# Kernel optimization log

Hardware: AMD Instinct MI355X
Metric: run time of the kernel (lower is better)

The kernel has to match this reference:

```python
import jax, jax.numpy as jnp
import numpy as np
import math

B, S, DIM = 2, 2048, 4096
N_HEADS, N_KV = 32, 8
HD = DIM // N_HEADS           # 128
N_REP = N_HEADS // N_KV       # 4
MAX_SEQ = 2048


def _rope_freqs(seq_len, head_dim):
    inv = 1.0 / (10000.0 ** (np.arange(0, head_dim, 2, dtype=np.float32) / head_dim))
    ang = np.outer(np.arange(seq_len, dtype=np.float32), inv)  # [S, HD/2]
    return jnp.asarray(np.cos(ang)), jnp.asarray(np.sin(ang))


def setup_inputs() -> dict:
    key = jax.random.key(0)
    ks = jax.random.split(key, 5)
    x = jax.random.normal(ks[0], (B, S, DIM), dtype=jnp.float32)
    wq = jax.random.normal(ks[1], (DIM, N_HEADS * HD), dtype=jnp.float32) * 0.02
    wk = jax.random.normal(ks[2], (DIM, N_KV * HD), dtype=jnp.float32) * 0.02
    wv = jax.random.normal(ks[3], (DIM, N_KV * HD), dtype=jnp.float32) * 0.02
    wo = jax.random.normal(ks[4], (N_HEADS * HD, DIM), dtype=jnp.float32) * 0.02
    freqs_cos, freqs_sin = _rope_freqs(S, HD)
    return {"x": x, "wq": wq, "wk": wk, "wv": wv, "wo": wo,
            "freqs_cos": freqs_cos, "freqs_sin": freqs_sin, "start_pos": 0}


def _apply_rope(t, cos, sin):
    # t: [B, S, H, HD]; adjacent pairs (2i, 2i+1) form complex numbers
    tr = t.reshape(*t.shape[:-1], HD // 2, 2)
    xr, xi = tr[..., 0], tr[..., 1]
    c = cos[None, :, None, :]  # [1, S, 1, HD/2]
    s = sin[None, :, None, :]
    o = jnp.stack([xr * c - xi * s, xr * s + xi * c], axis=-1)
    return o.reshape(t.shape)


def reference(x, wq, wk, wv, wo, freqs_cos, freqs_sin, start_pos):
    batch, seq_len, _ = x.shape
    q = (x @ wq).reshape(batch, seq_len, N_HEADS, HD)
    k = (x @ wk).reshape(batch, seq_len, N_KV, HD)
    v = (x @ wv).reshape(batch, seq_len, N_KV, HD)
    xq = _apply_rope(q, freqs_cos, freqs_sin)
    xk = _apply_rope(k, freqs_cos, freqs_sin)

    # KV-cache append (buffer initialized to zeros, as in the module)
    cache_k = jnp.zeros((batch, MAX_SEQ, N_KV, HD), dtype=x.dtype)
    cache_v = jnp.zeros((batch, MAX_SEQ, N_KV, HD), dtype=x.dtype)
    cache_k = jax.lax.dynamic_update_slice(cache_k, xk, (0, start_pos, 0, 0))
    cache_v = jax.lax.dynamic_update_slice(cache_v, v, (0, start_pos, 0, 0))
    keys = cache_k[:, : start_pos + seq_len]    # [B, T, KV, HD]
    values = cache_v[:, : start_pos + seq_len]

    # GQA: repeat kv heads n_rep times
    keys = jnp.repeat(keys, N_REP, axis=2)      # [B, T, H, HD]
    values = jnp.repeat(values, N_REP, axis=2)

    # [B, H, Sq, T] scores; no causal mask, matching the original module
    scores = jnp.einsum("bqhd,bkhd->bhqk", xq, keys) / math.sqrt(HD)
    attn = jax.nn.softmax(scores, axis=-1)
    out = jnp.einsum("bhqk,bkhd->bqhd", attn, values)
    out = out.reshape(batch, seq_len, N_HEADS * HD)
    return out @ wo
```

## Files before the change

kernel.cpp:

```cpp
#include <hip/hip_runtime.h>

#define S_LEN 2048

typedef __bf16 bf16x8 __attribute__((ext_vector_type(8)));
typedef float f32x4 __attribute__((ext_vector_type(4)));

static __device__ __forceinline__ unsigned short f32_to_bf16(float f){
  unsigned int u = __float_as_uint(f);
  u += 0x7FFFu + ((u >> 16) & 1u);
  return (unsigned short)(u >> 16);
}
static __device__ __forceinline__ float bf16_to_f32(unsigned short h){
  return __uint_as_float(((unsigned int)h) << 16);
}
static __device__ __forceinline__ bf16x8 ld_bf16x8(const unsigned short* p){
  return *reinterpret_cast<const bf16x8*>(p);
}
static __device__ __forceinline__ void async_copy16(const void* g, void* l){
  __builtin_amdgcn_global_load_lds(
      (const __attribute__((address_space(1))) void*)g,
      (__attribute__((address_space(3))) void*)l, 16, 0, 0);
}

__global__ void conv_f32_bf16(const float* __restrict__ in, unsigned short* __restrict__ out, int n4){
  int i = blockIdx.x * 256 + threadIdx.x;
  if (i >= n4) return;
  float4 v = ((const float4*)in)[i];
  ushort4 o;
  o.x = f32_to_bf16(v.x); o.y = f32_to_bf16(v.y);
  o.z = f32_to_bf16(v.z); o.w = f32_to_bf16(v.w);
  ((ushort4*)out)[i] = o;
}

__global__ void transpose_w(const float* __restrict__ in, unsigned short* __restrict__ out, int K, int N){
  __shared__ float tile[32][33];
  int n0 = blockIdx.x * 32, k0 = blockIdx.y * 32;
  int tx = threadIdx.x, ty = threadIdx.y;
  #pragma unroll
  for (int i=0;i<4;++i)
    tile[ty + i*8][tx] = in[(size_t)(k0 + ty + i*8) * N + n0 + tx];
  __syncthreads();
  #pragma unroll
  for (int i=0;i<4;++i)
    out[(size_t)(n0 + ty + i*8) * K + k0 + tx] = f32_to_bf16(tile[tx][ty + i*8]);
}

__global__ void rope_inplace(unsigned short* __restrict__ t, const float* __restrict__ cs,
                             const float* __restrict__ sn, int heads, float scale){
  int idx = blockIdx.x * 256 + threadIdx.x;
  int j = idx & 63;
  int tmp = idx >> 6;
  int h = tmp & (heads - 1);
  int row = tmp / heads;
  int s = row & (S_LEN - 1);
  float c = cs[s*64 + j], si = sn[s*64 + j];
  size_t base = (((size_t)row * heads + h) << 7) + (j << 1);
  float xr = bf16_to_f32(t[base]);
  float xi = bf16_to_f32(t[base + 1]);
  t[base]     = f32_to_bf16((xr * c - xi * si) * scale);
  t[base + 1] = f32_to_bf16((xr * si + xi * c) * scale);
}

template<bool OUT_BF16>
__global__ __launch_bounds__(256, 2) void gemm_bt(
    const unsigned short* __restrict__ A,
    const unsigned short* __restrict__ Bt,
    void* __restrict__ Cout, int N, int K)
{
  __shared__ alignas(16) unsigned short Asm[128 * 32];
  __shared__ alignas(16) unsigned short Bsm[128 * 32];
  const int tid  = threadIdx.x;
  const int wave = tid >> 6;
  const int lane = tid & 63;
  const int lm = lane & 15;
  const int kq = lane >> 4;
  const int wm = (wave >> 1) * 64;
  const int wn = (wave & 1) * 64;
  const size_t bm = (size_t)blockIdx.y * 128;
  const size_t bn = (size_t)blockIdx.x * 128;

  const f32x4 zero4 = {0.f, 0.f, 0.f, 0.f};
  f32x4 acc[4][4];
  #pragma unroll
  for (int i=0;i<4;++i)
    #pragma unroll
    for (int j=0;j<4;++j) acc[i][j] = zero4;

  const int srow = lane >> 2;
  const int sc   = ((lane & 3) ^ ((lane >> 3) & 3)) * 8;
  const unsigned short* gA0 = A  + (bm + wave*32      + srow) * (size_t)K + sc;
  const unsigned short* gA1 = A  + (bm + wave*32 + 16 + srow) * (size_t)K + sc;
  const unsigned short* gB0 = Bt + (bn + wave*32      + srow) * (size_t)K + sc;
  const unsigned short* gB1 = Bt + (bn + wave*32 + 16 + srow) * (size_t)K + sc;
  unsigned short* lA0 = &Asm[(wave*32     ) * 32];
  unsigned short* lA1 = &Asm[(wave*32 + 16) * 32];
  unsigned short* lB0 = &Bsm[(wave*32     ) * 32];
  unsigned short* lB1 = &Bsm[(wave*32 + 16) * 32];

  const int p8 = (kq ^ ((lm >> 1) & 3)) * 8;

  for (int k0 = 0; k0 < K; k0 += 32){
    async_copy16(gA0, lA0);
    async_copy16(gA1, lA1);
    async_copy16(gB0, lB0);
    async_copy16(gB1, lB1);
    gA0 += 32; gA1 += 32; gB0 += 32; gB1 += 32;
    __syncthreads();

    bf16x8 af[4], bfr[4];
    #pragma unroll
    for (int i=0;i<4;++i){
      af[i]  = ld_bf16x8(&Asm[(wm + i*16 + lm)*32 + p8]);
      bfr[i] = ld_bf16x8(&Bsm[(wn + i*16 + lm)*32 + p8]);
    }
    #pragma unroll
    for (int mi=0; mi<4; ++mi)
      #pragma unroll
      for (int ni=0; ni<4; ++ni)
        acc[mi][ni] = __builtin_amdgcn_mfma_f32_16x16x32_bf16(af[mi], bfr[ni], acc[mi][ni], 0, 0, 0);
    __syncthreads();
  }

  #pragma unroll
  for (int mi=0; mi<4; ++mi){
    #pragma unroll
    for (int ni=0; ni<4; ++ni){
      #pragma unroll
      for (int r=0; r<4; ++r){
        size_t row = bm + wm + mi*16 + kq*4 + r;
        size_t col = bn + wn + ni*16 + lm;
        if constexpr (OUT_BF16)
          ((unsigned short*)Cout)[row * N + col] = f32_to_bf16(acc[mi][ni][r]);
        else
          ((float*)Cout)[row * N + col] = acc[mi][ni][r];
      }
    }
  }
}

#define PP 72

__global__ __launch_bounds__(256, 2) void flash_attn(
    const unsigned short* __restrict__ Q,
    const unsigned short* __restrict__ Kc,
    const unsigned short* __restrict__ VT,
    unsigned short* __restrict__ O)
{
  __shared__ alignas(16) unsigned short Ksm[64 * 128];
  __shared__ alignas(16) unsigned short VTsm[128 * 64];
  __shared__ alignas(16) unsigned short Psm[4 * 32 * PP];

  const int tid  = threadIdx.x;
  const int wave = tid >> 6;
  const int lane = tid & 63;
  const int lm = lane & 15;
  const int kq = lane >> 4;
  const int b   = blockIdx.z;
  const int h   = blockIdx.y;
  const int kvh = h >> 2;
  const int q0  = blockIdx.x * 128;

  bf16x8 qf[2][4];
  #pragma unroll
  for (int mt=0; mt<2; ++mt){
    const size_t qbase = (((size_t)(b * S_LEN + q0 + mt*64 + wave*16 + lm)) * 32 + h) * 128;
    #pragma unroll
    for (int kf=0; kf<4; ++kf)
      qf[mt][kf] = ld_bf16x8(&Q[qbase + kf*32 + kq*8]);
  }

  const f32x4 zero4 = {0.f,0.f,0.f,0.f};
  f32x4 Oacc[2][8];
  #pragma unroll
  for (int mt=0; mt<2; ++mt)
    #pragma unroll
    for (int i=0;i<8;++i) Oacc[mt][i] = zero4;
  f32x4 lacc[2] = {zero4, zero4};

  union { unsigned short s[8]; bf16x8 v; } ou;
  #pragma unroll
  for (int i=0;i<8;++i) ou.s[i] = 0x3F80;
  const bf16x8 ones = ou.v;

  const unsigned short* Kg = Kc + (size_t)b * S_LEN * 1024 + (size_t)kvh * 128;
  const unsigned short* Vg = VT + (size_t)kvh * 128 * 4096 + (size_t)b * S_LEN;
  unsigned short* Pw = &Psm[wave * 32 * PP];

  const int kkey_in = lane >> 4;
  const int kccp    = lane & 15;
  const int vd_in   = lane >> 3;
  const int vchl    = ((lane & 7) ^ (vd_in & 7)) * 8;

  for (int kt = 0; kt < S_LEN/64; ++kt){
    #pragma unroll
    for (int c=0;c<4;++c){
      int kb4 = (wave*4 + c) * 4;
      int key = kb4 + kkey_in;
      int ccl = kccp ^ (key & 7);
      async_copy16(Kg + (size_t)(kt*64 + key) * 1024 + ccl*8, &Ksm[kb4 * 128]);
    }
    #pragma unroll
    for (int c=0;c<4;++c){
      int d0 = (wave*4 + c) * 8;
      int d  = d0 + vd_in;
      async_copy16(Vg + (size_t)d * 4096 + kt*64 + vchl, &VTsm[d0 * 64]);
    }
    __syncthreads();

    f32x4 sacc[2][4];
    #pragma unroll
    for (int nt=0;nt<4;++nt){ sacc[0][nt] = zero4; sacc[1][nt] = zero4; }
    #pragma unroll
    for (int nt=0; nt<4; ++nt){
      const int n = nt*16 + lm;
      #pragma unroll
      for (int kf=0; kf<4; ++kf){
        int pc = ((kf*4 + kq) ^ (lm & 7)) * 8;
        bf16x8 kfrag = ld_bf16x8(&Ksm[n*128 + pc]);
        sacc[0][nt] = __builtin_amdgcn_mfma_f32_16x16x32_bf16(qf[0][kf], kfrag, sacc[0][nt], 0,0,0);
        sacc[1][nt] = __builtin_amdgcn_mfma_f32_16x16x32_bf16(qf[1][kf], kfrag, sacc[1][nt], 0,0,0);
      }
    }

    #pragma unroll
    for (int mt=0; mt<2; ++mt){
      #pragma unroll
      for (int nt=0; nt<4; ++nt){
        #pragma unroll
        for (int e=0; e<4; ++e){
          float p = __expf(sacc[mt][nt][e]);
          Pw[(mt*16 + kq*4 + e)*PP + nt*16 + lm] = f32_to_bf16(p);
        }
      }
    }

    #pragma unroll
    for (int kf2=0; kf2<2; ++kf2){
      bf16x8 pf0 = ld_bf16x8(&Pw[(     lm)*PP + kf2*32 + kq*8]);
      bf16x8 pf1 = ld_bf16x8(&Pw[(16 + lm)*PP + kf2*32 + kq*8]);
      lacc[0] = __builtin_amdgcn_mfma_f32_16x16x32_bf16(pf0, ones, lacc[0], 0,0,0);
      lacc[1] = __builtin_amdgcn_mfma_f32_16x16x32_bf16(pf1, ones, lacc[1], 0,0,0);
      #pragma unroll
      for (int dt=0; dt<8; ++dt){
        int pc = ((kf2*4 + kq) ^ (lm & 7)) * 8;
        bf16x8 vfr = ld_bf16x8(&VTsm[(dt*16 + lm)*64 + pc]);
        Oacc[0][dt] = __builtin_amdgcn_mfma_f32_16x16x32_bf16(pf0, vfr, Oacc[0][dt], 0,0,0);
        Oacc[1][dt] = __builtin_amdgcn_mfma_f32_16x16x32_bf16(pf1, vfr, Oacc[1][dt], 0,0,0);
      }
    }
    __syncthreads();
  }

  #pragma unroll
  for (int mt=0; mt<2; ++mt){
    float inv[4];
    #pragma unroll
    for (int r=0;r<4;++r) inv[r] = __builtin_amdgcn_rcpf(lacc[mt][r]);
    const size_t obase = (((size_t)(b * S_LEN + q0 + mt*64 + wave*16 + kq*4)) * 32 + h) * 128;
    #pragma unroll
    for (int r=0;r<4;++r){
      #pragma unroll
      for (int dt=0; dt<8; ++dt)
        O[obase + (size_t)r * 4096 + dt*16 + lm] = f32_to_bf16(Oacc[mt][dt][r] * inv[r]);
    }
  }
}

extern "C" void kernel_launch(void* const* d_in, const int* in_sizes, int n_in,
                              void* d_out, int out_size, void* d_ws, size_t ws_size,
                              hipStream_t stream)
{
  const float* x    = (const float*)d_in[0];
  const float* wq   = (const float*)d_in[1];
  const float* wk   = (const float*)d_in[2];
  const float* wv   = (const float*)d_in[3];
  const float* wo   = (const float*)d_in[4];
  const float* fcos = (const float*)d_in[5];
  const float* fsin = (const float*)d_in[6];

  float* out = (float*)d_out;
  char* w = (char*)d_ws;
  const size_t MB = 1ull << 20;
  unsigned short* xb   = (unsigned short*)(w + 0);
  unsigned short* wqT  = (unsigned short*)(w + 32*MB);
  unsigned short* wkT  = (unsigned short*)(w + 64*MB);
  unsigned short* wvT  = (unsigned short*)(w + 72*MB);
  unsigned short* woT  = (unsigned short*)(w + 80*MB);
  unsigned short* qb   = (unsigned short*)(w + 112*MB);
  unsigned short* kb   = (unsigned short*)(w + 144*MB);
  unsigned short* vT   = (unsigned short*)(w + 152*MB);
  unsigned short* attn = (unsigned short*)(w + 0);

  conv_f32_bf16<<<dim3(16384), dim3(256), 0, stream>>>(x, xb, 4194304);

  transpose_w<<<dim3(128,128), dim3(32,8), 0, stream>>>(wq, wqT, 4096, 4096);
  transpose_w<<<dim3(32,128),  dim3(32,8), 0, stream>>>(wk, wkT, 4096, 1024);
  transpose_w<<<dim3(32,128),  dim3(32,8), 0, stream>>>(wv, wvT, 4096, 1024);
  transpose_w<<<dim3(128,128), dim3(32,8), 0, stream>>>(wo, woT, 4096, 4096);

  gemm_bt<true><<<dim3(32,32), dim3(256), 0, stream>>>(xb, wqT, qb, 4096, 4096);
  gemm_bt<true><<<dim3(8,32),  dim3(256), 0, stream>>>(xb, wkT, kb, 1024, 4096);
  gemm_bt<true><<<dim3(32,8),  dim3(256), 0, stream>>>(wvT, xb, vT, 4096, 4096);

  rope_inplace<<<dim3(32768), dim3(256), 0, stream>>>(qb, fcos, fsin, 32, 0.08838834764831845f);
  rope_inplace<<<dim3(8192),  dim3(256), 0, stream>>>(kb, fcos, fsin, 8, 1.0f);

  flash_attn<<<dim3(16, 32, 2), dim3(256), 0, stream>>>(qb, kb, vT, attn);

  gemm_bt<false><<<dim3(32,32), dim3(256), 0, stream>>>(attn, woT, out, 4096, 4096);
}
```

Before: 877.2 us.

## Fuse Q/K/V projections into one GEMM with a packed QKV buffer

Concatenates the transposed Wq, Wk and Wv into a single 6144-wide weight and runs one GEMM producing a packed QKV activation with row stride 6144. RoPE and flash attention now index into this packed buffer, and a new transpose kernel builds the V-transposed layout from the V slice. This replaces three GEMM launches with one larger, better-filled grid, including the V GEMM that previously ran on a 32x8 grid. In exchange it adds an extra transpose pass over V and strided K/Q loads.

Result: faster. 812.8 us (-7.3%).

```diff
diff --git a/kernel.cpp b/kernel.cpp
--- a/kernel.cpp
+++ b/kernel.cpp
@@ -43,6 +43,20 @@
   #pragma unroll
   for (int i=0;i<4;++i)
     out[(size_t)(n0 + ty + i*8) * K + k0 + tx] = f32_to_bf16(tile[tx][ty + i*8]);
+}
+
+__global__ void transpose_v(const unsigned short* __restrict__ in, unsigned short* __restrict__ out){
+  __shared__ unsigned short tile[32][33];
+  int r0 = blockIdx.x * 32;
+  int c0 = blockIdx.y * 32;
+  int tx = threadIdx.x, ty = threadIdx.y;
+  #pragma unroll
+  for (int i=0;i<4;++i)
+    tile[ty + i*8][tx] = in[(size_t)(r0 + ty + i*8) * 6144 + 5120 + c0 + tx];
+  __syncthreads();
+  #pragma unroll
+  for (int i=0;i<4;++i)
+    out[(size_t)(c0 + ty + i*8) * 4096 + r0 + tx] = tile[tx][ty + i*8];
 }
 
 __global__ void rope_inplace(unsigned short* __restrict__ t, const float* __restrict__ cs,
@@ -54,7 +68,7 @@
   int row = tmp / heads;
   int s = row & (S_LEN - 1);
   float c = cs[s*64 + j], si = sn[s*64 + j];
-  size_t base = (((size_t)row * heads + h) << 7) + (j << 1);
+  size_t base = (size_t)row * 6144 + (h << 7) + (j << 1);
   float xr = bf16_to_f32(t[base]);
   float xi = bf16_to_f32(t[base + 1]);
   t[base]     = f32_to_bf16((xr * c - xi * si) * scale);
@@ -139,10 +153,10 @@
 }
 
 #define PP 72
+#define QKV_STRIDE 6144
 
 __global__ __launch_bounds__(256, 2) void flash_attn(
-    const unsigned short* __restrict__ Q,
-    const unsigned short* __restrict__ Kc,
+    const unsigned short* __restrict__ QKV,
     const unsigned short* __restrict__ VT,
     unsigned short* __restrict__ O)
 {
@@ -163,10 +177,10 @@
   bf16x8 qf[2][4];
   #pragma unroll
   for (int mt=0; mt<2; ++mt){
-    const size_t qbase = (((size_t)(b * S_LEN + q0 + mt*64 + wave*16 + lm)) * 32 + h) * 128;
+    const size_t qbase = (size_t)(b * S_LEN + q0 + mt*64 + wave*16 + lm) * QKV_STRIDE + h * 128;
     #pragma unroll
     for (int kf=0; kf<4; ++kf)
-      qf[mt][kf] = ld_bf16x8(&Q[qbase + kf*32 + kq*8]);
+      qf[mt][kf] = ld_bf16x8(&QKV[qbase + kf*32 + kq*8]);
   }
 
   const f32x4 zero4 = {0.f,0.f,0.f,0.f};
@@ -182,7 +196,7 @@
   for (int i=0;i<8;++i) ou.s[i] = 0x3F80;
   const bf16x8 ones = ou.v;
 
-  const unsigned short* Kg = Kc + (size_t)b * S_LEN * 1024 + (size_t)kvh * 128;
+  const unsigned short* Kg = QKV + 4096 + (size_t)kvh * 128 + (size_t)b * S_LEN * QKV_STRIDE;
   const unsigned short* Vg = VT + (size_t)kvh * 128 * 4096 + (size_t)b * S_LEN;
   unsigned short* Pw = &Psm[wave * 32 * PP];
 
@@ -197,7 +211,7 @@
       int kb4 = (wave*4 + c) * 4;
       int key = kb4 + kkey_in;
       int ccl = kccp ^ (key & 7);
-      async_copy16(Kg + (size_t)(kt*64 + key) * 1024 + ccl*8, &Ksm[kb4 * 128]);
+      async_copy16(Kg + (size_t)(kt*64 + key) * QKV_STRIDE + ccl*8, &Ksm[kb4 * 128]);
     }
     #pragma unroll
     for (int c=0;c<4;++c){
@@ -281,31 +295,28 @@
   float* out = (float*)d_out;
   char* w = (char*)d_ws;
   const size_t MB = 1ull << 20;
-  unsigned short* xb   = (unsigned short*)(w + 0);
-  unsigned short* wqT  = (unsigned short*)(w + 32*MB);
-  unsigned short* wkT  = (unsigned short*)(w + 64*MB);
-  unsigned short* wvT  = (unsigned short*)(w + 72*MB);
-  unsigned short* woT  = (unsigned short*)(w + 80*MB);
-  unsigned short* qb   = (unsigned short*)(w + 112*MB);
-  unsigned short* kb   = (unsigned short*)(w + 144*MB);
-  unsigned short* vT   = (unsigned short*)(w + 152*MB);
-  unsigned short* attn = (unsigned short*)(w + 0);
+  unsigned short* xb    = (unsigned short*)(w + 0);
+  unsigned short* wqkvT = (unsigned short*)(w + 32*MB);
+  unsigned short* woT   = (unsigned short*)(w + 80*MB);
+  unsigned short* qkv   = (unsigned short*)(w + 112*MB);
+  unsigned short* vT    = (unsigned short*)(w + 32*MB);
+  unsigned short* attn  = (unsigned short*)(w + 0);
 
   conv_f32_bf16<<<dim3(16384), dim3(256), 0, stream>>>(x, xb, 4194304);
 
-  transpose_w<<<dim3(128,128), dim3(32,8), 0, stream>>>(wq, wqT, 4096, 4096);
-  transpose_w<<<dim3(32,128),  dim3(32,8), 0, stream>>>(wk, wkT, 4096, 1024);
-  transpose_w<<<dim3(32,128),  dim3(32,8), 0, stream>>>(wv, wvT, 4096, 1024);
+  transpose_w<<<dim3(128,128), dim3(32,8), 0, stream>>>(wq, wqkvT,                      4096, 4096);
+  transpose_w<<<dim3(32,128),  dim3(32,8), 0, stream>>>(wk, wqkvT + (size_t)4096*4096, 4096, 1024);
+  transpose_w<<<dim3(32,128),  dim3(32,8), 0, stream>>>(wv, wqkvT + (size_t)5120*4096, 4096, 1024);
   transpose_w<<<dim3(128,128), dim3(32,8), 0, stream>>>(wo, woT, 4096, 4096);
 
-  gemm_bt<true><<<dim3(32,32), dim3(256), 0, stream>>>(xb, wqT, qb, 4096, 4096);
-  gemm_bt<true><<<dim3(8,32),  dim3(256), 0, stream>>>(xb, wkT, kb, 1024, 4096);
-  gemm_bt<true><<<dim3(32,8),  dim3(256), 0, stream>>>(wvT, xb, vT, 4096, 4096);
-
-  rope_inplace<<<dim3(32768), dim3(256), 0, stream>>>(qb, fcos, fsin, 32, 0.08838834764831845f);
-  rope_inplace<<<dim3(8192),  dim3(256), 0, stream>>>(kb, fcos, fsin, 8, 1.0f);
-
-  flash_attn<<<dim3(16, 32, 2), dim3(256), 0, stream>>>(qb, kb, vT, attn);
+  gemm_bt<true><<<dim3(48,32), dim3(256), 0, stream>>>(xb, wqkvT, qkv, 6144, 4096);
+
+  rope_inplace<<<dim3(32768), dim3(256), 0, stream>>>(qkv,        fcos, fsin, 32, 0.08838834764831845f);
+  rope_inplace<<<dim3(8192),  dim3(256), 0, stream>>>(qkv + 4096, fcos, fsin, 8, 1.0f);
+
+  transpose_v<<<dim3(128,32), dim3(32,8), 0, stream>>>(qkv, vT);
+
+  flash_attn<<<dim3(16, 32, 2), dim3(256), 0, stream>>>(qkv, vT, attn);
 
   gemm_bt<false><<<dim3(32,32), dim3(256), 0, stream>>>(attn, woT, out, 4096, 4096);
 }
```
